# Kernel optimization log

Hardware: AMD Instinct MI355X
Metric: run time of the kernel (lower is better)

The kernel has to match this reference:

```python
import jax, jax.numpy as jnp
import numpy as np

B = 2048
LF = 64
N_DEC, N_MOV, N_CAT, N_PER, N_COM = 12, 60000, 32, 100000, 20000


def setup_inputs() -> dict:
    key = jax.random.key(0)
    ks = jax.random.split(key, 10)

    def multihot(k, n):
        return jax.random.randint(k, (B, n), 0, 2, dtype=jnp.int32)

    def weight(k, n):
        # nn.Linear(n, LF, bias=False) weight, stored transposed as [n, LF]
        return jax.random.normal(k, (n, LF), dtype=jnp.float32) * 0.02

    return {
        "decade_idxs": multihot(ks[0], N_DEC),
        "movie_idxs": multihot(ks[1], N_MOV),
        "category_idxs": multihot(ks[2], N_CAT),
        "person_idxs": multihot(ks[3], N_PER),
        "company_idxs": multihot(ks[4], N_COM),
        "W_dec": weight(ks[5], N_DEC),
        "W_mov": weight(ks[6], N_MOV),
        "W_cat": weight(ks[7], N_CAT),
        "W_per": weight(ks[8], N_PER),
        "W_com": weight(ks[9], N_COM),
    }


def _norm_rows(emb, s):
    # divide rows whose multi-hot sum s is nonzero (np.flatnonzero semantics)
    mask = s != 0
    safe = jnp.where(mask, s, jnp.ones_like(s))
    return jnp.where(mask[:, None], emb / safe[:, None], emb)


def reference(decade_idxs, movie_idxs, category_idxs, person_idxs, company_idxs,
              W_dec, W_mov, W_cat, W_per, W_com):
    d = decade_idxs.astype(jnp.float32)
    m = movie_idxs.astype(jnp.float32)
    c = category_idxs.astype(jnp.float32)
    p = person_idxs.astype(jnp.float32)
    q = company_idxs.astype(jnp.float32)

    decades = d @ W_dec            # [B, LF]
    decades = _norm_rows(decades, jnp.sum(d, axis=1))

    movies = m @ W_mov
    # BUG in original module (replicated faithfully): `decades` is normalized
    # AGAIN by the movie-row sums; `movies` is never normalized.
    decades = _norm_rows(decades, jnp.sum(m, axis=1))

    categories = _norm_rows(c @ W_cat, jnp.sum(c, axis=1))
    persons = _norm_rows(p @ W_per, jnp.sum(p, axis=1))
    companies = _norm_rows(q @ W_com, jnp.sum(q, axis=1))

    return jnp.concatenate([decades, movies, categories, persons, companies], axis=1)
```

## Files before the change

### kernel.cpp

```cpp
#include <hip/hip_runtime.h>
#include <hip/hip_bf16.h>

#define LF 64
#define NBAGS 5
#define BROWS 2048
#define OUTC 320
#define KC 2048
#define MT_BLOCK 128
#define NMT (BROWS / MT_BLOCK)

#define WS_SUMS_BYTES 65536
#define WP_BYTES 23068672ull
#define PART_OFF (WS_SUMS_BYTES + WP_BYTES)
#define NCHUNKS 90
#define PART_BYTES ((size_t)NCHUNKS * BROWS * LF * 4)

typedef __attribute__((ext_vector_type(8))) short short8;
typedef __attribute__((ext_vector_type(4))) float f32x4;

struct BagArgs {
    const int*   A[NBAGS];
    const float* W[NBAGS];
    int K[NBAGS];
    int cstart[NBAGS + 1];
    int tstart[NBAGS + 1];
};

__device__ __forceinline__ unsigned short f2bf(float f) {
    unsigned u = __float_as_uint(f);
    u += 0x7FFFu + ((u >> 16) & 1u);
    return (unsigned short)(u >> 16);
}

__global__ __launch_bounds__(256) void pack_w(BagArgs args,
                                              unsigned short* __restrict__ Wp) {
    __shared__ unsigned short ls[4][4096];
    const int wv = threadIdx.x >> 6;
    const int c  = threadIdx.x & 63;
    const int gtile = blockIdx.x * 4 + wv;

    int bag = 0;
#pragma unroll
    for (int b = 1; b < NBAGS; ++b)
        if (gtile >= args.tstart[b]) bag = b;
    const int lt = gtile - args.tstart[bag];
    const float* __restrict__ W = args.W[bag];
    const int K = args.K[bag];

    unsigned short* L = ls[wv];
#pragma unroll 8
    for (int k = 0; k < 64; ++k) {
        const int gk = lt * 64 + k;
        float v = (gk < K) ? W[(size_t)gk * LF + c] : 0.f;
        L[(((k >> 3) * LF) + c) * 8 + (k & 7)] = f2bf(v);
    }
    __syncthreads();
    unsigned short* dst = Wp + ((size_t)gtile << 12);
#pragma unroll
    for (int j = 0; j < 8; ++j)
        *(short8*)(dst + c * 8 + j * 512) = *(const short8*)(L + c * 8 + j * 512);
}

template<int MODE>
__global__ __launch_bounds__(256) void bag_gemm(BagArgs args,
                                                const unsigned short* __restrict__ Wp,
                                                float* __restrict__ dstbuf,
                                                int* __restrict__ sums)
{
    const int tid  = threadIdx.x;
    const int wave = tid >> 6;
    const int lane = tid & 63;
    const int fr   = lane & 15;
    const int kg   = lane >> 4;

    const int g  = blockIdx.x >> 4;
    const int mt = blockIdx.x & 15;

    int bag = 1;
#pragma unroll
    for (int b = 2; b < NBAGS; ++b)
        if (g >= args.cstart[b]) bag = b;
    const int chunk  = g - args.cstart[bag];
    const int K      = args.K[bag];
    const int kc0    = chunk * KC;
    const int nsteps = (min(kc0 + KC, K) - kc0) >> 5;

    const int row0 = mt * MT_BLOCK + wave * 32;
    const int* __restrict__ pA0 = args.A[bag] + (size_t)(row0 + fr) * K + kc0 + kg * 8;
    const int* __restrict__ pA1 = pA0 + (size_t)16 * K;
    const unsigned short* __restrict__ pB =
        Wp + ((size_t)(args.tstart[bag] + chunk * (KC / 64)) << 12) + (kg * LF + fr) * 8;
    const float* __restrict__ Wf = args.W[bag];

    f32x4 acc0[4], acc1[4];
#pragma unroll
    for (int i = 0; i < 4; ++i) {
        acc0[i] = (f32x4){0.f, 0.f, 0.f, 0.f};
        acc1[i] = (f32x4){0.f, 0.f, 0.f, 0.f};
    }
    int psum0 = 0, psum1 = 0;

    auto loadA = [&](int s, int4 (&x)[4]) {
        const int* p0 = pA0 + s * 32;
        const int* p1 = pA1 + s * 32;
        x[0] = *(const int4*)(p0);
        x[1] = *(const int4*)(p0 + 4);
        x[2] = *(const int4*)(p1);
        x[3] = *(const int4*)(p1 + 4);
    };
    auto loadB = [&](int s, short8 (&y)[4]) {
        if constexpr (MODE < 2) {
            const unsigned short* p = pB + (size_t)s * 2048;
            y[0] = *(const short8*)(p);
            y[1] = *(const short8*)(p + 128);
            y[2] = *(const short8*)(p + 256);
            y[3] = *(const short8*)(p + 384);
        } else {
            const int kb = kc0 + s * 32 + kg * 8;
#pragma unroll
            for (int ni = 0; ni < 4; ++ni) {
                unsigned short t[8];
#pragma unroll
                for (int j = 0; j < 8; ++j)
                    t[j] = f2bf(Wf[(size_t)(kb + j) * LF + ni * 16 + fr]);
                y[ni] = *(short8*)t;
            }
        }
    };
    auto compute = [&](const int4 (&x)[4], const short8 (&y)[4]) {
        psum0 += x[0].x + x[0].y + x[0].z + x[0].w
               + x[1].x + x[1].y + x[1].z + x[1].w;
        psum1 += x[2].x + x[2].y + x[2].z + x[2].w
               + x[3].x + x[3].y + x[3].z + x[3].w;
        const unsigned q0 = (unsigned)(x[0].x | (x[0].y << 16)) * 0x3F80u;
        const unsigned q1 = (unsigned)(x[0].z | (x[0].w << 16)) * 0x3F80u;
        const unsigned q2 = (unsigned)(x[1].x | (x[1].y << 16)) * 0x3F80u;
        const unsigned q3 = (unsigned)(x[1].z | (x[1].w << 16)) * 0x3F80u;
        const unsigned q4 = (unsigned)(x[2].x | (x[2].y << 16)) * 0x3F80u;
        const unsigned q5 = (unsigned)(x[2].z | (x[2].w << 16)) * 0x3F80u;
        const unsigned q6 = (unsigned)(x[3].x | (x[3].y << 16)) * 0x3F80u;
        const unsigned q7 = (unsigned)(x[3].z | (x[3].w << 16)) * 0x3F80u;
        int4 u0 = make_int4((int)q0, (int)q1, (int)q2, (int)q3);
        int4 u1 = make_int4((int)q4, (int)q5, (int)q6, (int)q7);
        short8 fa0 = *(short8*)&u0;
        short8 fa1 = *(short8*)&u1;
#pragma unroll
        for (int ni = 0; ni < 4; ++ni) {
            acc0[ni] = __builtin_amdgcn_mfma_f32_16x16x32_bf16(fa0, y[ni], acc0[ni], 0, 0, 0);
            acc1[ni] = __builtin_amdgcn_mfma_f32_16x16x32_bf16(fa1, y[ni], acc1[ni], 0, 0, 0);
        }
    };

    int4   Aa[4], Ab[4];
    short8 Ba[4], Bb[4];
    loadA(0, Aa);
    loadB(0, Ba);
    const int npair = (nsteps + 1) >> 1;
    for (int p = 0; p < npair; ++p) {
        const int s1  = 2 * p + 1;
        const int s1c = min(s1, nsteps - 1);
        loadA(s1c, Ab);
        loadB(s1c, Bb);
        __builtin_amdgcn_sched_barrier(0);
        compute(Aa, Ba);
        const int s2c = min(2 * p + 2, nsteps - 1);
        loadA(s2c, Aa);
        loadB(s2c, Ba);
        __builtin_amdgcn_sched_barrier(0);
        if (s1 < nsteps)
            compute(Ab, Bb);
    }

    psum0 += __shfl_xor(psum0, 16);
    psum0 += __shfl_xor(psum0, 32);
    psum1 += __shfl_xor(psum1, 16);
    psum1 += __shfl_xor(psum1, 32);
    if (kg == 0) {
        atomicAdd(&sums[bag * BROWS + row0 + fr], psum0);
        atomicAdd(&sums[bag * BROWS + row0 + 16 + fr], psum1);
    }

    if constexpr (MODE == 0) {
        float* dst = dstbuf + ((size_t)g * BROWS + row0 + kg * 4) * LF + fr;
#pragma unroll
        for (int ni = 0; ni < 4; ++ni)
#pragma unroll
            for (int r = 0; r < 4; ++r) {
                dst[(size_t)(r) * LF + ni * 16]      = acc0[ni][r];
                dst[(size_t)(16 + r) * LF + ni * 16] = acc1[ni][r];
            }
    } else {
#pragma unroll
        for (int ni = 0; ni < 4; ++ni)
#pragma unroll
            for (int r = 0; r < 4; ++r) {
                atomicAdd(dstbuf + (size_t)(row0 + kg * 4 + r) * OUTC + bag * LF + ni * 16 + fr,
                          acc0[ni][r]);
                atomicAdd(dstbuf + (size_t)(row0 + 16 + kg * 4 + r) * OUTC + bag * LF + ni * 16 + fr,
                          acc1[ni][r]);
            }
    }
}

template<bool FROMPART>
__global__ __launch_bounds__(256) void reduce_norm(BagArgs args,
                                                   const float* __restrict__ part,
                                                   float* __restrict__ out,
                                                   const int* __restrict__ sums)
{
    const int idx = blockIdx.x * 256 + threadIdx.x;
    if (idx >= BROWS * OUTC) return;
    const int row = idx / OUTC;
    const int c   = idx - row * OUTC;
    const int bag = c >> 6;
    const int col = c & 63;

    float v;
    if (bag == 0) {
        const int*   A0 = args.A[0];
        const float* W0 = args.W[0];
        float a = 0.f; int s = 0;
#pragma unroll
        for (int k = 0; k < 12; ++k) {
            const int x = A0[row * 12 + k];
            s += x;
            if (x) a += W0[k * LF + col];
        }
        if (s) a /= (float)s;
        const int sm = sums[1 * BROWS + row];
        if (sm) a /= (float)sm;
        v = a;
    } else {
        if constexpr (FROMPART) {
            float a = 0.f;
            for (int gg = args.cstart[bag]; gg < args.cstart[bag + 1]; ++gg)
                a += part[((size_t)gg * BROWS + row) * LF + col];
            v = a;
        } else {
            v = out[idx];
        }
        if (bag >= 2) {
            const int s = sums[bag * BROWS + row];
            if (s) v /= (float)s;
        }
    }
    out[idx] = v;
}

extern "C" void kernel_launch(void* const* d_in, const int* in_sizes, int n_in,
                              void* d_out, int out_size, void* d_ws, size_t ws_size,
                              hipStream_t stream) {
    float* out = (float*)d_out;
    int* sums = (int*)d_ws;
    unsigned short* Wp = (unsigned short*)((char*)d_ws + WS_SUMS_BYTES);
    float* part = (float*)((char*)d_ws + PART_OFF);

    BagArgs args;
    const int Ks[NBAGS] = {12, 60000, 32, 100000, 20000};
    int tcum = 0;
    for (int b = 0; b < NBAGS; ++b) {
        args.A[b] = (const int*)d_in[b];
        args.W[b] = (const float*)d_in[5 + b];
        args.K[b] = Ks[b];
        args.tstart[b] = tcum;
        tcum += (Ks[b] + 63) / 64;
    }
    args.tstart[NBAGS] = tcum;
    args.cstart[0] = 0;
    int ccum = 0;
    for (int b = 1; b < NBAGS; ++b) {
        args.cstart[b] = ccum;
        ccum += (Ks[b] + KC - 1) / KC;
    }
    args.cstart[NBAGS] = ccum;

    hipMemsetAsync(sums, 0, NBAGS * BROWS * sizeof(int), stream);

    const bool have_wp   = ws_size >= (size_t)WS_SUMS_BYTES + WP_BYTES;
    const bool have_part = ws_size >= PART_OFF + PART_BYTES;

    if (have_wp)
        pack_w<<<tcum / 4, 256, 0, stream>>>(args, Wp);

    dim3 grid(NCHUNKS * NMT);
    if (have_wp && have_part) {
        bag_gemm<0><<<grid, 256, 0, stream>>>(args, Wp, part, sums);
        reduce_norm<true><<<(BROWS * OUTC + 255) / 256, 256, 0, stream>>>(args, part, out, sums);
    } else if (have_wp) {
        hipMemsetAsync(d_out, 0, (size_t)out_size * sizeof(float), stream);
        bag_gemm<1><<<grid, 256, 0, stream>>>(args, Wp, out, sums);
        reduce_norm<false><<<(BROWS * OUTC + 255) / 256, 256, 0, stream>>>(args, part, out, sums);
    } else {
        hipMemsetAsync(d_out, 0, (size_t)out_size * sizeof(float), stream);
        bag_gemm<2><<<grid, 256, 0, stream>>>(args, Wp, out, sums);
        reduce_norm<false><<<(BROWS * OUTC + 255) / 256, 256, 0, stream>>>(args, part, out, sums);
    }
}
```

Before: 406.9 us.

## Compute row sums via MFMA with ones, widen A loads to 16 contiguous ints

Row sums of the multi-hot inputs are now computed with extra MFMA instructions against a ones vector instead of scalar integer adds plus shuffles, and the sums buffer becomes float. Each lane now loads 16 contiguous A ints per step over 64-wide super-steps, with the packed weight layout reordered to match. A masked path handles K tails that are not multiples of 64. The aim is to cut VALU work and improve load width. In exchange it adds MFMA work for the sums and relies on float atomics, which stay exact for integer sums this small.

```diff
diff --git a/kernel.cpp b/kernel.cpp
--- a/kernel.cpp
+++ b/kernel.cpp
@@ -1,5 +1,6 @@
 #include <hip/hip_runtime.h>
 #include <hip/hip_bf16.h>
+#include <type_traits>
 
 #define LF 64
 #define NBAGS 5
@@ -52,7 +53,8 @@
     for (int k = 0; k < 64; ++k) {
         const int gk = lt * 64 + k;
         float v = (gk < K) ? W[(size_t)gk * LF + c] : 0.f;
-        L[(((k >> 3) * LF) + c) * 8 + (k & 7)] = f2bf(v);
+        const int block = ((k >> 3) & 1) * 4 + (k >> 4);
+        L[(block * LF + c) * 8 + (k & 7)] = f2bf(v);
     }
     __syncthreads();
     unsigned short* dst = Wp + ((size_t)gtile << 12);
@@ -65,7 +67,7 @@
 __global__ __launch_bounds__(256) void bag_gemm(BagArgs args,
                                                 const unsigned short* __restrict__ Wp,
                                                 float* __restrict__ dstbuf,
-                                                int* __restrict__ sums)
+                                                float* __restrict__ sums)
 {
     const int tid  = threadIdx.x;
     const int wave = tid >> 6;
@@ -83,10 +85,12 @@
     const int chunk  = g - args.cstart[bag];
     const int K      = args.K[bag];
     const int kc0    = chunk * KC;
-    const int nsteps = (min(kc0 + KC, K) - kc0) >> 5;
+    const int kend   = min(kc0 + KC, K);
+    const int ksz    = kend - kc0;
+    const int nsuper = (ksz + 63) >> 6;
 
     const int row0 = mt * MT_BLOCK + wave * 32;
-    const int* __restrict__ pA0 = args.A[bag] + (size_t)(row0 + fr) * K + kc0 + kg * 8;
+    const int* __restrict__ pA0 = args.A[bag] + (size_t)(row0 + fr) * K + kc0 + kg * 16;
     const int* __restrict__ pA1 = pA0 + (size_t)16 * K;
     const unsigned short* __restrict__ pB =
         Wp + ((size_t)(args.tstart[bag] + chunk * (KC / 64)) << 12) + (kg * LF + fr) * 8;
@@ -98,86 +102,118 @@
         acc0[i] = (f32x4){0.f, 0.f, 0.f, 0.f};
         acc1[i] = (f32x4){0.f, 0.f, 0.f, 0.f};
     }
-    int psum0 = 0, psum1 = 0;
-
-    auto loadA = [&](int s, int4 (&x)[4]) {
-        const int* p0 = pA0 + s * 32;
-        const int* p1 = pA1 + s * 32;
-        x[0] = *(const int4*)(p0);
-        x[1] = *(const int4*)(p0 + 4);
-        x[2] = *(const int4*)(p1);
-        x[3] = *(const int4*)(p1 + 4);
+    f32x4 accS0 = (f32x4){0.f, 0.f, 0.f, 0.f};
+    f32x4 accS1 = (f32x4){0.f, 0.f, 0.f, 0.f};
+    const int4 uo = make_int4(0x3F803F80, 0x3F803F80, 0x3F803F80, 0x3F803F80);
+    const short8 ones = *(const short8*)&uo;
+
+    auto loadB = [&](int ss, short8 (&y)[2][4]) {
+        if constexpr (MODE < 2) {
+            const unsigned short* p = pB + (size_t)ss * 4096;
+#pragma unroll
+            for (int m = 0; m < 2; ++m)
+#pragma unroll
+                for (int ni = 0; ni < 4; ++ni)
+                    y[m][ni] = *(const short8*)(p + m * 2048 + ni * 128);
+        } else {
+#pragma unroll
+            for (int m = 0; m < 2; ++m)
+#pragma unroll
+                for (int ni = 0; ni < 4; ++ni) {
+                    unsigned short t[8];
+#pragma unroll
+                    for (int j = 0; j < 8; ++j) {
+                        const int kq = kc0 + ss * 64 + kg * 16 + m * 8 + j;
+                        t[j] = (kq < kend) ? f2bf(Wf[(size_t)kq * LF + ni * 16 + fr]) : 0;
+                    }
+                    y[m][ni] = *(short8*)t;
+                }
+        }
     };
-    auto loadB = [&](int s, short8 (&y)[4]) {
-        if constexpr (MODE < 2) {
-            const unsigned short* p = pB + (size_t)s * 2048;
-            y[0] = *(const short8*)(p);
-            y[1] = *(const short8*)(p + 128);
-            y[2] = *(const short8*)(p + 256);
-            y[3] = *(const short8*)(p + 384);
-        } else {
-            const int kb = kc0 + s * 32 + kg * 8;
+
+    auto compute = [&](const int4 (&x)[8], const short8 (&y)[2][4]) {
+        short8 fa[2][2];
+#pragma unroll
+        for (int rs = 0; rs < 2; ++rs)
+#pragma unroll
+            for (int m = 0; m < 2; ++m) {
+                const int4& a = x[rs * 4 + m * 2];
+                const int4& b = x[rs * 4 + m * 2 + 1];
+                const unsigned q0 = (unsigned)(a.x | (a.y << 16)) * 0x3F80u;
+                const unsigned q1 = (unsigned)(a.z | (a.w << 16)) * 0x3F80u;
+                const unsigned q2 = (unsigned)(b.x | (b.y << 16)) * 0x3F80u;
+                const unsigned q3 = (unsigned)(b.z | (b.w << 16)) * 0x3F80u;
+                int4 u = make_int4((int)q0, (int)q1, (int)q2, (int)q3);
+                fa[rs][m] = *(short8*)&u;
+            }
+#pragma unroll
+        for (int m = 0; m < 2; ++m) {
+            accS0 = __builtin_amdgcn_mfma_f32_16x16x32_bf16(fa[0][m], ones, accS0, 0, 0, 0);
+            accS1 = __builtin_amdgcn_mfma_f32_16x16x32_bf16(fa[1][m], ones, accS1, 0, 0, 0);
 #pragma unroll
             for (int ni = 0; ni < 4; ++ni) {
-                unsigned short t[8];
-#pragma unroll
-                for (int j = 0; j < 8; ++j)
-                    t[j] = f2bf(Wf[(size_t)(kb + j) * LF + ni * 16 + fr]);
-                y[ni] = *(short8*)t;
+                acc0[ni] = __builtin_amdgcn_mfma_f32_16x16x32_bf16(fa[0][m], y[m][ni], acc0[ni], 0, 0, 0);
+                acc1[ni] = __builtin_amdgcn_mfma_f32_16x16x32_bf16(fa[1][m], y[m][ni], acc1[ni], 0, 0, 0);
             }
         }
     };
-    auto compute = [&](const int4 (&x)[4], const short8 (&y)[4]) {
-        psum0 += x[0].x + x[0].y + x[0].z + x[0].w
-               + x[1].x + x[1].y + x[1].z + x[1].w;
-        psum1 += x[2].x + x[2].y + x[2].z + x[2].w
-               + x[3].x + x[3].y + x[3].z + x[3].w;
-        const unsigned q0 = (unsigned)(x[0].x | (x[0].y << 16)) * 0x3F80u;
-        const unsigned q1 = (unsigned)(x[0].z | (x[0].w << 16)) * 0x3F80u;
-        const unsigned q2 = (unsigned)(x[1].x | (x[1].y << 16)) * 0x3F80u;
-        const unsigned q3 = (unsigned)(x[1].z | (x[1].w << 16)) * 0x3F80u;
-        const unsigned q4 = (unsigned)(x[2].x | (x[2].y << 16)) * 0x3F80u;
-        const unsigned q5 = (unsigned)(x[2].z | (x[2].w << 16)) * 0x3F80u;
-        const unsigned q6 = (unsigned)(x[3].x | (x[3].y << 16)) * 0x3F80u;
-        const unsigned q7 = (unsigned)(x[3].z | (x[3].w << 16)) * 0x3F80u;
-        int4 u0 = make_int4((int)q0, (int)q1, (int)q2, (int)q3);
-        int4 u1 = make_int4((int)q4, (int)q5, (int)q6, (int)q7);
-        short8 fa0 = *(short8*)&u0;
-        short8 fa1 = *(short8*)&u1;
-#pragma unroll
-        for (int ni = 0; ni < 4; ++ni) {
-            acc0[ni] = __builtin_amdgcn_mfma_f32_16x16x32_bf16(fa0, y[ni], acc0[ni], 0, 0, 0);
-            acc1[ni] = __builtin_amdgcn_mfma_f32_16x16x32_bf16(fa1, y[ni], acc1[ni], 0, 0, 0);
+
+    auto pipeline = [&](auto MASKED) {
+        auto loadA = [&](int ss, int4 (&x)[8]) {
+            if constexpr (decltype(MASKED)::value) {
+#pragma unroll
+                for (int i = 0; i < 4; ++i) {
+                    const int kq = kc0 + ss * 64 + kg * 16 + i * 4;
+                    const int kcl = min(kq, kend - 4);
+                    const int d = kcl - kq;
+                    int4 v0 = *(const int4*)(pA0 + ss * 64 + i * 4 + d);
+                    int4 v1 = *(const int4*)(pA1 + ss * 64 + i * 4 + d);
+                    const bool ok = kq < kend;
+                    const int4 z = make_int4(0, 0, 0, 0);
+                    x[i]     = ok ? v0 : z;
+                    x[4 + i] = ok ? v1 : z;
+                }
+            } else {
+                const int* p0 = pA0 + ss * 64;
+                const int* p1 = pA1 + ss * 64;
+#pragma unroll
+                for (int i = 0; i < 4; ++i) {
+                    x[i]     = *(const int4*)(p0 + i * 4);
+                    x[4 + i] = *(const int4*)(p1 + i * 4);
+                }
+            }
+        };
+
+        int4   Aa[8], Ab[8];
+        short8 Ba[2][4], Bb[2][4];
+        loadA(0, Aa);
+        loadB(0, Ba);
+        const int npair = (nsuper + 1) >> 1;
+        for (int p = 0; p < npair; ++p) {
+            const int s1  = 2 * p + 1;
+            const int s1c = min(s1, nsuper - 1);
+            loadA(s1c, Ab);
+            loadB(s1c, Bb);
+            __builtin_amdgcn_sched_barrier(0);
+            compute(Aa, Ba);
+            const int s2c = min(2 * p + 2, nsuper - 1);
+            loadA(s2c, Aa);
+            loadB(s2c, Ba);
+            __builtin_amdgcn_sched_barrier(0);
+            if (s1 < nsuper)
+                compute(Ab, Bb);
         }
     };
 
-    int4   Aa[4], Ab[4];
-    short8 Ba[4], Bb[4];
-    loadA(0, Aa);
-    loadB(0, Ba);
-    const int npair = (nsteps + 1) >> 1;
-    for (int p = 0; p < npair; ++p) {
-        const int s1  = 2 * p + 1;
-        const int s1c = min(s1, nsteps - 1);
-        loadA(s1c, Ab);
-        loadB(s1c, Bb);
-        __builtin_amdgcn_sched_barrier(0);
-        compute(Aa, Ba);
-        const int s2c = min(2 * p + 2, nsteps - 1);
-        loadA(s2c, Aa);
-        loadB(s2c, Ba);
-        __builtin_amdgcn_sched_barrier(0);
-        if (s1 < nsteps)
-            compute(Ab, Bb);
-    }
-
-    psum0 += __shfl_xor(psum0, 16);
-    psum0 += __shfl_xor(psum0, 32);
-    psum1 += __shfl_xor(psum1, 16);
-    psum1 += __shfl_xor(psum1, 32);
-    if (kg == 0) {
-        atomicAdd(&sums[bag * BROWS + row0 + fr], psum0);
-        atomicAdd(&sums[bag * BROWS + row0 + 16 + fr], psum1);
+    if ((ksz & 63) == 0) pipeline(std::false_type{});
+    else                 pipeline(std::true_type{});
+
+    if (fr == 0) {
+#pragma unroll
+        for (int r = 0; r < 4; ++r) {
+            atomicAdd(&sums[bag * BROWS + row0 + kg * 4 + r],      accS0[r]);
+            atomicAdd(&sums[bag * BROWS + row0 + 16 + kg * 4 + r], accS1[r]);
+        }
     }
 
     if constexpr (MODE == 0) {
@@ -206,7 +242,7 @@
 __global__ __launch_bounds__(256) void reduce_norm(BagArgs args,
                                                    const float* __restrict__ part,
                                                    float* __restrict__ out,
-                                                   const int* __restrict__ sums)
+                                                   const float* __restrict__ sums)
 {
     const int idx = blockIdx.x * 256 + threadIdx.x;
     if (idx >= BROWS * OUTC) return;
@@ -227,8 +263,8 @@
             if (x) a += W0[k * LF + col];
         }
         if (s) a /= (float)s;
-        const int sm = sums[1 * BROWS + row];
-        if (sm) a /= (float)sm;
+        const float sm = sums[1 * BROWS + row];
+        if (sm != 0.f) a /= sm;
         v = a;
     } else {
         if constexpr (FROMPART) {
@@ -240,8 +276,8 @@
             v = out[idx];
         }
         if (bag >= 2) {
-            const int s = sums[bag * BROWS + row];
-            if (s) v /= (float)s;
+            const float s = sums[bag * BROWS + row];
+            if (s != 0.f) v /= s;
         }
     }
     out[idx] = v;
@@ -251,7 +287,7 @@
                               void* d_out, int out_size, void* d_ws, size_t ws_size,
                               hipStream_t stream) {
     float* out = (float*)d_out;
-    int* sums = (int*)d_ws;
+    float* sums = (float*)d_ws;
     unsigned short* Wp = (unsigned short*)((char*)d_ws + WS_SUMS_BYTES);
     float* part = (float*)((char*)d_ws + PART_OFF);
 
@@ -274,7 +310,7 @@
     }
     args.cstart[NBAGS] = ccum;
 
-    hipMemsetAsync(sums, 0, NBAGS * BROWS * sizeof(int), stream);
+    hipMemsetAsync(sums, 0, NBAGS * BROWS * sizeof(float), stream);
 
     const bool have_wp   = ws_size >= (size_t)WS_SUMS_BYTES + WP_BYTES;
     const bool have_part = ws_size >= PART_OFF + PART_BYTES;
```

Measured after the change: 452.9 us. 11.3% more time.

## Stage A and packed W tiles into LDS via async global_load_lds double buffering

Applied to the files above, without the earlier changes.

The bag GEMM now streams the int32 multi-hot A tiles and packed bf16 W tiles straight into a double-buffered LDS area with global_load_lds, working through 64-wide K super-steps with a waitcnt and barrier pipeline. It no longer loads directly into registers. The W packing layout is reordered to match the new LDS read pattern, and tail columns point at a zeroed workspace region. The aim is to hide global-memory latency for the bandwidth-bound 0/1 matrix stream. The cost is 80 KB of LDS per block, which lowers occupancy, plus extra block barriers. The fallback modes are replaced by a single naive kernel for small workspaces.

```diff
diff --git a/kernel.cpp b/kernel.cpp
--- a/kernel.cpp
+++ b/kernel.cpp
@@ -8,15 +8,19 @@
 #define KC 2048
 #define MT_BLOCK 128
 #define NMT (BROWS / MT_BLOCK)
-
-#define WS_SUMS_BYTES 65536
+#define NCHUNKS 90
+
+#define WS_HEAD 65536
+#define ZP_OFF 49152
 #define WP_BYTES 23068672ull
-#define PART_OFF (WS_SUMS_BYTES + WP_BYTES)
-#define NCHUNKS 90
+#define PART_OFF (WS_HEAD + WP_BYTES)
 #define PART_BYTES ((size_t)NCHUNKS * BROWS * LF * 4)
 
 typedef __attribute__((ext_vector_type(8))) short short8;
 typedef __attribute__((ext_vector_type(4))) float f32x4;
+
+typedef const __attribute__((address_space(1))) void gas_t;
+typedef __attribute__((address_space(3))) void las_t;
 
 struct BagArgs {
     const int*   A[NBAGS];
@@ -52,7 +56,8 @@
     for (int k = 0; k < 64; ++k) {
         const int gk = lt * 64 + k;
         float v = (gk < K) ? W[(size_t)gk * LF + c] : 0.f;
-        L[(((k >> 3) * LF) + c) * 8 + (k & 7)] = f2bf(v);
+        const int block = ((k >> 3) & 1) * 4 + (k >> 4);
+        L[(block * LF + c) * 8 + (k & 7)] = f2bf(v);
     }
     __syncthreads();
     unsigned short* dst = Wp + ((size_t)gtile << 12);
@@ -61,12 +66,14 @@
         *(short8*)(dst + c * 8 + j * 512) = *(const short8*)(L + c * 8 + j * 512);
 }
 
-template<int MODE>
 __global__ __launch_bounds__(256) void bag_gemm(BagArgs args,
                                                 const unsigned short* __restrict__ Wp,
-                                                float* __restrict__ dstbuf,
+                                                const int* __restrict__ zp,
+                                                float* __restrict__ part,
                                                 int* __restrict__ sums)
 {
+    __shared__ char lds[2][40960];
+
     const int tid  = threadIdx.x;
     const int wave = tid >> 6;
     const int lane = tid & 63;
@@ -83,14 +90,32 @@
     const int chunk  = g - args.cstart[bag];
     const int K      = args.K[bag];
     const int kc0    = chunk * KC;
-    const int nsteps = (min(kc0 + KC, K) - kc0) >> 5;
+    const int kend   = min(kc0 + KC, K);
+    const int nsuper = (kend - kc0 + 63) >> 6;
+    const int tile0  = args.tstart[bag] + chunk * (KC / 64);
 
     const int row0 = mt * MT_BLOCK + wave * 32;
-    const int* __restrict__ pA0 = args.A[bag] + (size_t)(row0 + fr) * K + kc0 + kg * 8;
-    const int* __restrict__ pA1 = pA0 + (size_t)16 * K;
-    const unsigned short* __restrict__ pB =
-        Wp + ((size_t)(args.tstart[bag] + chunk * (KC / 64)) << 12) + (kg * LF + fr) * 8;
-    const float* __restrict__ Wf = args.W[bag];
+    const int* __restrict__ Abase = args.A[bag];
+
+    auto stage = [&](int ss, int bufi) {
+        char* dA = &lds[bufi][0] + wave * 8192;
+#pragma unroll
+        for (int i = 0; i < 8; ++i) {
+            const int rs = i & 1, j = i >> 1;
+            const int col = kc0 + ss * 64 + kg * 16 + j * 4;
+            const int row = row0 + rs * 16 + fr;
+            const int* src = Abase + (size_t)row * K + col;
+            if (col >= kend) src = zp;
+            __builtin_amdgcn_global_load_lds((gas_t*)src, (las_t*)(dA + i * 1024),
+                                             16, 0, 0);
+        }
+        const char* sB = (const char*)Wp + ((size_t)(tile0 + ss) << 13)
+                         + wave * 2048 + lane * 16;
+        char* dB = &lds[bufi][32768] + wave * 2048;
+        __builtin_amdgcn_global_load_lds((gas_t*)sB, (las_t*)dB, 16, 0, 0);
+        __builtin_amdgcn_global_load_lds((gas_t*)(sB + 1024), (las_t*)(dB + 1024),
+                                         16, 0, 0);
+    };
 
     f32x4 acc0[4], acc1[4];
 #pragma unroll
@@ -98,111 +123,69 @@
         acc0[i] = (f32x4){0.f, 0.f, 0.f, 0.f};
         acc1[i] = (f32x4){0.f, 0.f, 0.f, 0.f};
     }
-    int psum0 = 0, psum1 = 0;
-
-    auto loadA = [&](int s, int4 (&x)[4]) {
-        const int* p0 = pA0 + s * 32;
-        const int* p1 = pA1 + s * 32;
-        x[0] = *(const int4*)(p0);
-        x[1] = *(const int4*)(p0 + 4);
-        x[2] = *(const int4*)(p1);
-        x[3] = *(const int4*)(p1 + 4);
-    };
-    auto loadB = [&](int s, short8 (&y)[4]) {
-        if constexpr (MODE < 2) {
-            const unsigned short* p = pB + (size_t)s * 2048;
-            y[0] = *(const short8*)(p);
-            y[1] = *(const short8*)(p + 128);
-            y[2] = *(const short8*)(p + 256);
-            y[3] = *(const short8*)(p + 384);
-        } else {
-            const int kb = kc0 + s * 32 + kg * 8;
+    int ps0 = 0, ps1 = 0;
+
+    stage(0, 0);
+    if (nsuper > 1) stage(1, 1);
+
+    for (int ss = 0; ss < nsuper; ++ss) {
+        const int cur = ss & 1;
+        if (ss + 1 < nsuper) asm volatile("s_waitcnt vmcnt(10)" ::: "memory");
+        else                 asm volatile("s_waitcnt vmcnt(0)"  ::: "memory");
+        __builtin_amdgcn_sched_barrier(0);
+        __builtin_amdgcn_s_barrier();
+
+        const char* Ab = &lds[cur][0]     + wave * 8192 + kg * 256 + fr * 16;
+        const char* Bb = &lds[cur][32768] + kg * 1024 + fr * 16;
+
+        short8 fa[2][2];
+#pragma unroll
+        for (int m = 0; m < 2; ++m)
+#pragma unroll
+            for (int rs = 0; rs < 2; ++rs) {
+                int4 lo = *(const int4*)(Ab + (size_t)(4 * m + rs) * 1024);
+                int4 hi = *(const int4*)(Ab + (size_t)(4 * m + 2 + rs) * 1024);
+                const int s = lo.x + lo.y + lo.z + lo.w + hi.x + hi.y + hi.z + hi.w;
+                if (rs == 0) ps0 += s; else ps1 += s;
+                const unsigned q0 = (unsigned)(lo.x | (lo.y << 16)) * 0x3F80u;
+                const unsigned q1 = (unsigned)(lo.z | (lo.w << 16)) * 0x3F80u;
+                const unsigned q2 = (unsigned)(hi.x | (hi.y << 16)) * 0x3F80u;
+                const unsigned q3 = (unsigned)(hi.z | (hi.w << 16)) * 0x3F80u;
+                int4 u = make_int4((int)q0, (int)q1, (int)q2, (int)q3);
+                fa[rs][m] = *(short8*)&u;
+            }
+#pragma unroll
+        for (int m = 0; m < 2; ++m)
 #pragma unroll
             for (int ni = 0; ni < 4; ++ni) {
-                unsigned short t[8];
-#pragma unroll
-                for (int j = 0; j < 8; ++j)
-                    t[j] = f2bf(Wf[(size_t)(kb + j) * LF + ni * 16 + fr]);
-                y[ni] = *(short8*)t;
+                const short8 y = *(const short8*)(Bb + m * 4096 + ni * 256);
+                acc0[ni] = __builtin_amdgcn_mfma_f32_16x16x32_bf16(fa[0][m], y, acc0[ni], 0, 0, 0);
+                acc1[ni] = __builtin_amdgcn_mfma_f32_16x16x32_bf16(fa[1][m], y, acc1[ni], 0, 0, 0);
             }
-        }
-    };
-    auto compute = [&](const int4 (&x)[4], const short8 (&y)[4]) {
-        psum0 += x[0].x + x[0].y + x[0].z + x[0].w
-               + x[1].x + x[1].y + x[1].z + x[1].w;
-        psum1 += x[2].x + x[2].y + x[2].z + x[2].w
-               + x[3].x + x[3].y + x[3].z + x[3].w;
-        const unsigned q0 = (unsigned)(x[0].x | (x[0].y << 16)) * 0x3F80u;
-        const unsigned q1 = (unsigned)(x[0].z | (x[0].w << 16)) * 0x3F80u;
-        const unsigned q2 = (unsigned)(x[1].x | (x[1].y << 16)) * 0x3F80u;
-        const unsigned q3 = (unsigned)(x[1].z | (x[1].w << 16)) * 0x3F80u;
-        const unsigned q4 = (unsigned)(x[2].x | (x[2].y << 16)) * 0x3F80u;
-        const unsigned q5 = (unsigned)(x[2].z | (x[2].w << 16)) * 0x3F80u;
-        const unsigned q6 = (unsigned)(x[3].x | (x[3].y << 16)) * 0x3F80u;
-        const unsigned q7 = (unsigned)(x[3].z | (x[3].w << 16)) * 0x3F80u;
-        int4 u0 = make_int4((int)q0, (int)q1, (int)q2, (int)q3);
-        int4 u1 = make_int4((int)q4, (int)q5, (int)q6, (int)q7);
-        short8 fa0 = *(short8*)&u0;
-        short8 fa1 = *(short8*)&u1;
-#pragma unroll
-        for (int ni = 0; ni < 4; ++ni) {
-            acc0[ni] = __builtin_amdgcn_mfma_f32_16x16x32_bf16(fa0, y[ni], acc0[ni], 0, 0, 0);
-            acc1[ni] = __builtin_amdgcn_mfma_f32_16x16x32_bf16(fa1, y[ni], acc1[ni], 0, 0, 0);
-        }
-    };
-
-    int4   Aa[4], Ab[4];
-    short8 Ba[4], Bb[4];
-    loadA(0, Aa);
-    loadB(0, Ba);
-    const int npair = (nsteps + 1) >> 1;
-    for (int p = 0; p < npair; ++p) {
-        const int s1  = 2 * p + 1;
-        const int s1c = min(s1, nsteps - 1);
-        loadA(s1c, Ab);
-        loadB(s1c, Bb);
-        __builtin_amdgcn_sched_barrier(0);
-        compute(Aa, Ba);
-        const int s2c = min(2 * p + 2, nsteps - 1);
-        loadA(s2c, Aa);
-        loadB(s2c, Ba);
-        __builtin_amdgcn_sched_barrier(0);
-        if (s1 < nsteps)
-            compute(Ab, Bb);
-    }
-
-    psum0 += __shfl_xor(psum0, 16);
-    psum0 += __shfl_xor(psum0, 32);
-    psum1 += __shfl_xor(psum1, 16);
-    psum1 += __shfl_xor(psum1, 32);
+
+        __builtin_amdgcn_s_barrier();
+        if (ss + 2 < nsuper) stage(ss + 2, cur);
+    }
+
+    ps0 += __shfl_xor(ps0, 16);
+    ps0 += __shfl_xor(ps0, 32);
+    ps1 += __shfl_xor(ps1, 16);
+    ps1 += __shfl_xor(ps1, 32);
     if (kg == 0) {
-        atomicAdd(&sums[bag * BROWS + row0 + fr], psum0);
-        atomicAdd(&sums[bag * BROWS + row0 + 16 + fr], psum1);
-    }
-
-    if constexpr (MODE == 0) {
-        float* dst = dstbuf + ((size_t)g * BROWS + row0 + kg * 4) * LF + fr;
-#pragma unroll
-        for (int ni = 0; ni < 4; ++ni)
-#pragma unroll
-            for (int r = 0; r < 4; ++r) {
-                dst[(size_t)(r) * LF + ni * 16]      = acc0[ni][r];
-                dst[(size_t)(16 + r) * LF + ni * 16] = acc1[ni][r];
-            }
-    } else {
-#pragma unroll
-        for (int ni = 0; ni < 4; ++ni)
-#pragma unroll
-            for (int r = 0; r < 4; ++r) {
-                atomicAdd(dstbuf + (size_t)(row0 + kg * 4 + r) * OUTC + bag * LF + ni * 16 + fr,
-                          acc0[ni][r]);
-                atomicAdd(dstbuf + (size_t)(row0 + 16 + kg * 4 + r) * OUTC + bag * LF + ni * 16 + fr,
-                          acc1[ni][r]);
-            }
-    }
-}
-
-template<bool FROMPART>
+        atomicAdd(&sums[bag * BROWS + row0 + fr], ps0);
+        atomicAdd(&sums[bag * BROWS + row0 + 16 + fr], ps1);
+    }
+
+    float* dst = part + ((size_t)g * BROWS + row0 + kg * 4) * LF + fr;
+#pragma unroll
+    for (int ni = 0; ni < 4; ++ni)
+#pragma unroll
+        for (int r = 0; r < 4; ++r) {
+            dst[(size_t)(r) * LF + ni * 16]      = acc0[ni][r];
+            dst[(size_t)(16 + r) * LF + ni * 16] = acc1[ni][r];
+        }
+}
+
 __global__ __launch_bounds__(256) void reduce_norm(BagArgs args,
                                                    const float* __restrict__ part,
                                                    float* __restrict__ out,
@@ -231,20 +214,41 @@
         if (sm) a /= (float)sm;
         v = a;
     } else {
-        if constexpr (FROMPART) {
-            float a = 0.f;
-            for (int gg = args.cstart[bag]; gg < args.cstart[bag + 1]; ++gg)
-                a += part[((size_t)gg * BROWS + row) * LF + col];
-            v = a;
-        } else {
-            v = out[idx];
-        }
+        float a = 0.f;
+        for (int gg = args.cstart[bag]; gg < args.cstart[bag + 1]; ++gg)
+            a += part[((size_t)gg * BROWS + row) * LF + col];
+        v = a;
         if (bag >= 2) {
             const int s = sums[bag * BROWS + row];
             if (s) v /= (float)s;
         }
     }
     out[idx] = v;
+}
+
+__global__ void naive_bag(BagArgs args, float* __restrict__ out) {
+    const int row = blockIdx.x;
+    const int c   = threadIdx.x;
+    if (c >= OUTC) return;
+    const int bag = c >> 6;
+    const int col = c & 63;
+    const int K = args.K[bag];
+    const int* A = args.A[bag] + (size_t)row * K;
+    const float* W = args.W[bag];
+    float a = 0.f; int s = 0;
+    for (int k = 0; k < K; ++k) {
+        const int x = A[k];
+        s += x;
+        if (x) a += W[(size_t)k * LF + col];
+    }
+    if (bag != 1 && s) a /= (float)s;
+    if (bag == 0) {
+        const int* A1 = args.A[1] + (size_t)row * args.K[1];
+        int sm = 0;
+        for (int k = 0; k < args.K[1]; ++k) sm += A1[k];
+        if (sm) a /= (float)sm;
+    }
+    out[(size_t)row * OUTC + c] = a;
 }
 
 extern "C" void kernel_launch(void* const* d_in, const int* in_sizes, int n_in,
@@ -252,7 +256,8 @@
                               hipStream_t stream) {
     float* out = (float*)d_out;
     int* sums = (int*)d_ws;
-    unsigned short* Wp = (unsigned short*)((char*)d_ws + WS_SUMS_BYTES);
+    const int* zp = (const int*)((const char*)d_ws + ZP_OFF);
+    unsigned short* Wp = (unsigned short*)((char*)d_ws + WS_HEAD);
     float* part = (float*)((char*)d_ws + PART_OFF);
 
     BagArgs args;
@@ -274,25 +279,15 @@
     }
     args.cstart[NBAGS] = ccum;
 
-    hipMemsetAsync(sums, 0, NBAGS * BROWS * sizeof(int), stream);
-
-    const bool have_wp   = ws_size >= (size_t)WS_SUMS_BYTES + WP_BYTES;
-    const bool have_part = ws_size >= PART_OFF + PART_BYTES;
-
-    if (have_wp)
-        pack_w<<<tcum / 4, 256, 0, stream>>>(args, Wp);
-
-    dim3 grid(NCHUNKS * NMT);
-    if (have_wp && have_part) {
-        bag_gemm<0><<<grid, 256, 0, stream>>>(args, Wp, part, sums);
-        reduce_norm<true><<<(BROWS * OUTC + 255) / 256, 256, 0, stream>>>(args, part, out, sums);
-    } else if (have_wp) {
-        hipMemsetAsync(d_out, 0, (size_t)out_size * sizeof(float), stream);
-        bag_gemm<1><<<grid, 256, 0, stream>>>(args, Wp, out, sums);
-        reduce_norm<false><<<(BROWS * OUTC + 255) / 256, 256, 0, stream>>>(args, part, out, sums);
-    } else {
-        hipMemsetAsync(d_out, 0, (size_t)out_size * sizeof(float), stream);
-        bag_gemm<2><<<grid, 256, 0, stream>>>(args, Wp, out, sums);
-        reduce_norm<false><<<(BROWS * OUTC + 255) / 256, 256, 0, stream>>>(args, part, out, sums);
-    }
-}
+    const bool ok = ws_size >= PART_OFF + PART_BYTES;
+    if (!ok) {
+        naive_bag<<<BROWS, OUTC, 0, stream>>>(args, out);
+        return;
+    }
+
+    hipMemsetAsync(d_ws, 0, WS_HEAD, stream);
+
+    pack_w<<<tcum / 4, 256, 0, stream>>>(args, Wp);
+    bag_gemm<<<NCHUNKS * NMT, 256, 0, stream>>>(args, Wp, zp, part, sums);
+    reduce_norm<<<(BROWS * OUTC + 255) / 256, 256, 0, stream>>>(args, part, out, sums);
+}
```

After: 458.5 us. 1.13x slower.
